# Kernel optimization log

Measured on AMD Instinct MI355X. Metric: run time of the kernel, lower is better.

Reference implementation:

```python
import jax, jax.numpy as jnp
import numpy as np

N_NODES = 50000
N_EDGES = 600000
IN_CH = 128
HID = 128
OUT_CH = 1
N_GRAPHS = 64


def setup_inputs() -> dict:
    key = jax.random.key(0)
    ks = jax.random.split(key, 16)
    inp = {
        "x": jax.random.normal(ks[0], (N_NODES, IN_CH), dtype=jnp.float32),
        "edge_index": jax.random.randint(ks[1], (2, N_EDGES), 0, N_NODES, dtype=jnp.int64),
        "edge_weight": jax.random.uniform(ks[2], (N_EDGES,), dtype=jnp.float32),
        "batch": jnp.sort(jax.random.randint(ks[3], (N_NODES,), 0, N_GRAPHS, dtype=jnp.int64)),
    }
    # SAGEConv params: lin_l (neighbor-aggregate path, has bias) and lin_r (root path)
    dims = [(IN_CH, HID), (HID, HID), (HID, HID), (HID, HID)]
    for i, (din, dout) in enumerate(dims, start=1):
        s = 1.0 / np.sqrt(din)
        inp[f"Wl{i}"] = jax.random.uniform(ks[3 + 2 * i], (din, dout), minval=-s, maxval=s, dtype=jnp.float32)
        inp[f"Wr{i}"] = jax.random.uniform(ks[4 + 2 * i], (din, dout), minval=-s, maxval=s, dtype=jnp.float32)
        inp[f"b{i}"] = jnp.zeros((dout,), dtype=jnp.float32)
    s = 1.0 / np.sqrt(HID)
    inp["Wc"] = jax.random.uniform(ks[14], (HID, OUT_CH), minval=-s, maxval=s, dtype=jnp.float32)
    inp["bc"] = jnp.zeros((OUT_CH,), dtype=jnp.float32)
    return inp


def _sage_conv(x, src, dst, Wl, Wr, b):
    # mean aggregation of source-node features at each destination node
    msg = x[src]  # [E, d] gather
    agg = jax.ops.segment_sum(msg, dst, num_segments=N_NODES)
    cnt = jax.ops.segment_sum(jnp.ones((src.shape[0],), x.dtype), dst, num_segments=N_NODES)
    agg = agg / jnp.maximum(cnt, 1.0)[:, None]
    return agg @ Wl + b + x @ Wr


def reference(x, edge_index, edge_weight, batch,
              Wl1, Wr1, b1, Wl2, Wr2, b2, Wl3, Wr3, b3, Wl4, Wr4, b4, Wc, bc):
    src, dst = edge_index[0], edge_index[1]
    h = jax.nn.relu(_sage_conv(x, src, dst, Wl1, Wr1, b1))
    h = jax.nn.relu(_sage_conv(h, src, dst, Wl2, Wr2, b2))
    h = jax.nn.relu(_sage_conv(h, src, dst, Wl3, Wr3, b3))
    h = jax.nn.relu(_sage_conv(h, src, dst, Wl4, Wr4, b4))
    # global mean pool over graphs
    pooled = jax.ops.segment_sum(h, batch, num_segments=N_GRAPHS)
    gcnt = jax.ops.segment_sum(jnp.ones((N_NODES,), h.dtype), batch, num_segments=N_GRAPHS)
    pooled = pooled / jnp.maximum(gcnt, 1.0)[:, None]  # [G, HID]
    return jax.nn.sigmoid(pooled @ Wc + bc)  # [G, 1]
```

## Files before the change

### kernel.cpp

```cpp
#include <hip/hip_runtime.h>
#include <math.h>

#define NND 50000
#define LNP 50048
#define NED 600000
#define CD  128
#define NG  64
#define NBLK 196
#define GROWS 64

typedef short s8v  __attribute__((ext_vector_type(8)));
typedef float f4v  __attribute__((ext_vector_type(4)));
typedef float f2v  __attribute__((ext_vector_type(2)));
typedef unsigned short u16x4 __attribute__((ext_vector_type(4)));
typedef unsigned short u16x8 __attribute__((ext_vector_type(8)));

static __device__ __forceinline__ unsigned short f2bf(float f) {
  union { float f; unsigned u; } v; v.f = f;
  unsigned r = v.u + 0x7fffu + ((v.u >> 16) & 1u);
  return (unsigned short)(r >> 16);
}
static __device__ __forceinline__ unsigned short f2bf_t(float f) {
  union { float f; unsigned u; } v; v.f = f;
  return (unsigned short)(v.u >> 16);
}
static __device__ __forceinline__ unsigned f2fp8x4(float a, float b, float c, float d) {
  int r = __builtin_amdgcn_cvt_pk_fp8_f32(a, b, 0, false);
  r = __builtin_amdgcn_cvt_pk_fp8_f32(c, d, r, true);
  return (unsigned)r;
}
static __device__ __forceinline__ s8v fp8x8_to_bf16(uint2 v) {
  f2v c0 = __builtin_amdgcn_cvt_pk_f32_fp8(v.x, false);
  f2v c1 = __builtin_amdgcn_cvt_pk_f32_fp8(v.x, true);
  f2v c2 = __builtin_amdgcn_cvt_pk_f32_fp8(v.y, false);
  f2v c3 = __builtin_amdgcn_cvt_pk_f32_fp8(v.y, true);
  union { u16x8 u; s8v s; } o;
  o.u[0] = f2bf_t(c0.x); o.u[1] = f2bf_t(c0.y);
  o.u[2] = f2bf_t(c1.x); o.u[3] = f2bf_t(c1.y);
  o.u[4] = f2bf_t(c2.x); o.u[5] = f2bf_t(c2.y);
  o.u[6] = f2bf_t(c3.x); o.u[7] = f2bf_t(c3.y);
  return o.s;
}
static __device__ __forceinline__ void g2lds8(const unsigned char* g, unsigned char* l) {
  __builtin_amdgcn_global_load_lds(
      (const __attribute__((address_space(1))) unsigned*)g,
      (__attribute__((address_space(3))) unsigned*)l, 16, 0, 0);
}

__global__ __launch_bounds__(256) void bsum_k(const int* __restrict__ cnt,
                                              int* __restrict__ bsum) {
  __shared__ int s[256];
  int i = blockIdx.x * 256 + threadIdx.x;
  s[threadIdx.x] = (i < NND) ? cnt[i] : 0;
  __syncthreads();
  for (int off = 128; off > 0; off >>= 1) {
    if (threadIdx.x < off) s[threadIdx.x] += s[threadIdx.x + off];
    __syncthreads();
  }
  if (threadIdx.x == 0) bsum[blockIdx.x] = s[0];
}

__global__ __launch_bounds__(256) void bscan_k(const int* __restrict__ bsum,
                                               int* __restrict__ boff,
                                               int* __restrict__ offs,
                                               const int* __restrict__ batch,
                                               int* __restrict__ gb) {
  __shared__ int s[256];
  int t = threadIdx.x;
  if (t <= NG) {
    int lo = 0, hi = NND;
    while (lo < hi) {
      int mid = (lo + hi) >> 1;
      if (batch[mid] < t) lo = mid + 1; else hi = mid;
    }
    gb[t] = lo;
  }
  s[t] = (t < NBLK) ? bsum[t] : 0;
  __syncthreads();
  for (int off = 1; off < 256; off <<= 1) {
    int v = (t >= off) ? s[t - off] : 0;
    __syncthreads();
    s[t] += v;
    __syncthreads();
  }
  if (t < NBLK) boff[t] = (t == 0) ? 0 : s[t - 1];
  if (t == NBLK - 1) offs[NND] = s[t];
}

__global__ __launch_bounds__(256) void escan_k(const int* __restrict__ cnt,
                                               const int* __restrict__ boff,
                                               int* __restrict__ offs,
                                               int* __restrict__ cur) {
  __shared__ int s[256];
  int i = blockIdx.x * 256 + threadIdx.x;
  int t = threadIdx.x;
  int v = (i < NND) ? cnt[i] : 0;
  s[t] = v;
  __syncthreads();
  for (int off = 1; off < 256; off <<= 1) {
    int u = (t >= off) ? s[t - off] : 0;
    __syncthreads();
    s[t] += u;
    __syncthreads();
  }
  if (i < NND) {
    int excl = s[t] - v + boff[blockIdx.x];
    offs[i] = excl;
    cur[i]  = excl;
  }
}

__global__ void fill_k(const int* __restrict__ src, const int* __restrict__ dst,
                       int* __restrict__ cur, int* __restrict__ csr) {
  int e = blockIdx.x * blockDim.x + threadIdx.x;
  if (e >= NED) return;
  int d = dst[e];
  int pos = atomicAdd(&cur[d], 1);
  csr[pos] = src[e];
}

struct WPtrs { const float* w[8]; unsigned short* wt[8]; };
__global__ void prep_k(const float* __restrict__ x, unsigned* __restrict__ x8,
                       WPtrs p, const int* __restrict__ dst, int* __restrict__ cnt) {
  int t = blockIdx.x * blockDim.x + threadIdx.x;
  if (t < NND * 32) {
    float4 v = reinterpret_cast<const float4*>(x)[t];
    x8[t] = f2fp8x4(v.x, v.y, v.z, v.w);
  } else {
    int u = t - NND * 32;
    if (u < 8 * CD * CD) {
      int m = u >> 14, r = u & (CD * CD - 1);
      int n = r >> 7, k = r & 127;
      p.wt[m][r] = f2bf(p.w[m][k * CD + n]);
    } else {
      int e = u - 8 * CD * CD;
      if (e < NED) atomicAdd(&cnt[dst[e]], 1);
    }
  }
}

__global__ __launch_bounds__(256, 4) void sage_k(
    const unsigned* __restrict__ xq,
    const int* __restrict__ csr, const int* __restrict__ offs,
    const unsigned short* __restrict__ WlT, const unsigned short* __restrict__ WrT,
    const float* __restrict__ bias, unsigned char* __restrict__ h8,
    const int* __restrict__ batch, float* __restrict__ pooled) {
  __shared__ unsigned short abuf[GROWS * CD];
  __shared__ unsigned char  x8buf[GROWS * CD];
  __shared__ int sB[GROWS];

  const int tid  = threadIdx.x;
  const int wave = tid >> 6;
  const int lane = tid & 63;
  const int quad = lane >> 4;
  const int l16  = lane & 15;
  const size_t rbase = (size_t)blockIdx.x * GROWS;

  {
    const unsigned char* xg = (const unsigned char*)xq;
#pragma unroll
    for (int j = 0; j < 2; ++j) {
      const int s = j * 256 + tid;
      g2lds8(xg + (rbase + (s >> 3)) * CD + (s & 7) * 16, &x8buf[(size_t)s * 16]);
    }
  }

  if (pooled && tid < GROWS) {
    size_t row = rbase + tid;
    sB[tid] = (row < NND) ? batch[row] : -1;
  }

  s8v bL[2][4], bR[2][4];
#pragma unroll
  for (int nt = 0; nt < 2; ++nt) {
    const int n = wave * 32 + nt * 16 + l16;
#pragma unroll
    for (int kk = 0; kk < 4; ++kk) {
      size_t woff = (size_t)n * CD + kk * 32 + quad * 8;
      bL[nt][kk] = *reinterpret_cast<const s8v*>(WlT + woff);
      bR[nt][kk] = *reinterpret_cast<const s8v*>(WrT + woff);
    }
  }
  const float bv0 = bias[wave * 32 + l16];
  const float bv1 = bias[wave * 32 + 16 + l16];

  {
    const int team = tid >> 3;
    const int tl   = tid & 7;
    const unsigned* base = xq + tl * 4;
    for (int i = 0; i < 2; ++i) {
      const int rl = team * 2 + i;
      const size_t row = rbase + rl;
      u16x8 o0 = {}, o1 = {};
      if (row < NND) {
        const int e0 = offs[row], e1 = offs[row + 1];
        f2v a[8] = {};
        int e = e0;
        for (; e + 4 <= e1; e += 4) {
          int s[4];
#pragma unroll
          for (int j = 0; j < 4; ++j) s[j] = csr[e + j];
          uint4 v[4];
#pragma unroll
          for (int j = 0; j < 4; ++j)
            v[j] = *reinterpret_cast<const uint4*>(base + (size_t)s[j] * 32);
#pragma unroll
          for (int j = 0; j < 4; ++j) {
            a[0] += __builtin_amdgcn_cvt_pk_f32_fp8(v[j].x, false);
            a[1] += __builtin_amdgcn_cvt_pk_f32_fp8(v[j].x, true);
            a[2] += __builtin_amdgcn_cvt_pk_f32_fp8(v[j].y, false);
            a[3] += __builtin_amdgcn_cvt_pk_f32_fp8(v[j].y, true);
            a[4] += __builtin_amdgcn_cvt_pk_f32_fp8(v[j].z, false);
            a[5] += __builtin_amdgcn_cvt_pk_f32_fp8(v[j].z, true);
            a[6] += __builtin_amdgcn_cvt_pk_f32_fp8(v[j].w, false);
            a[7] += __builtin_amdgcn_cvt_pk_f32_fp8(v[j].w, true);
          }
        }
        for (; e < e1; ++e) {
          uint4 v = *reinterpret_cast<const uint4*>(base + (size_t)csr[e] * 32);
          a[0] += __builtin_amdgcn_cvt_pk_f32_fp8(v.x, false);
          a[1] += __builtin_amdgcn_cvt_pk_f32_fp8(v.x, true);
          a[2] += __builtin_amdgcn_cvt_pk_f32_fp8(v.y, false);
          a[3] += __builtin_amdgcn_cvt_pk_f32_fp8(v.y, true);
          a[4] += __builtin_amdgcn_cvt_pk_f32_fp8(v.z, false);
          a[5] += __builtin_amdgcn_cvt_pk_f32_fp8(v.z, true);
          a[6] += __builtin_amdgcn_cvt_pk_f32_fp8(v.w, false);
          a[7] += __builtin_amdgcn_cvt_pk_f32_fp8(v.w, true);
        }
        const float invd = 1.0f / fmaxf((float)(e1 - e0), 1.0f);
#pragma unroll
        for (int c = 0; c < 4; ++c) {
          o0[2 * c]     = f2bf(a[c].x * invd);
          o0[2 * c + 1] = f2bf(a[c].y * invd);
          o1[2 * c]     = f2bf(a[4 + c].x * invd);
          o1[2 * c + 1] = f2bf(a[4 + c].y * invd);
        }
      }
      *reinterpret_cast<u16x8*>(abuf + rl * CD + tl * 16)     = o0;
      *reinterpret_cast<u16x8*>(abuf + rl * CD + tl * 16 + 8) = o1;
    }
  }

  __syncthreads();

  const bool fast = pooled && (rbase + GROWS <= NND) && (sB[0] == sB[GROWS - 1]);
  const int c0 = wave * 32 + l16;
  float p0 = 0.f, p1 = 0.f;

#pragma unroll
  for (int rt = 0; rt < GROWS / 16; ++rt) {
    const unsigned short* arow = abuf + (rt * 16 + l16) * CD + quad * 8;
    const unsigned char*  xrow = x8buf + (rt * 16 + l16) * CD + quad * 8;
    f4v acc0 = {}, acc1 = {};
#pragma unroll
    for (int kk = 0; kk < 4; ++kk) {
      s8v aA = *reinterpret_cast<const s8v*>(arow + kk * 32);
      s8v aX = fp8x8_to_bf16(*reinterpret_cast<const uint2*>(xrow + kk * 32));
      acc0 = __builtin_amdgcn_mfma_f32_16x16x32_bf16(aA, bL[0][kk], acc0, 0, 0, 0);
      acc0 = __builtin_amdgcn_mfma_f32_16x16x32_bf16(aX, bR[0][kk], acc0, 0, 0, 0);
      acc1 = __builtin_amdgcn_mfma_f32_16x16x32_bf16(aA, bL[1][kk], acc1, 0, 0, 0);
      acc1 = __builtin_amdgcn_mfma_f32_16x16x32_bf16(aX, bR[1][kk], acc1, 0, 0, 0);
    }
    const size_t row0 = rbase + rt * 16 + quad * 4;
#pragma unroll
    for (int r = 0; r < 4; ++r) {
      const size_t row = row0 + r;
      float v0 = fmaxf(acc0[r] + bv0, 0.0f);
      float v1 = fmaxf(acc1[r] + bv1, 0.0f);
      if (h8) {
        int q0 = __builtin_amdgcn_cvt_pk_fp8_f32(v0, v0, 0, false);
        int q1 = __builtin_amdgcn_cvt_pk_fp8_f32(v1, v1, 0, false);
        h8[row * CD + c0]      = (unsigned char)q0;
        h8[row * CD + c0 + 16] = (unsigned char)q1;
      }
      if (pooled) {
        if (fast) {
          p0 += v0; p1 += v1;
        } else {
          int g = sB[rt * 16 + quad * 4 + r];
          if (g >= 0) {
            atomicAdd(&pooled[g * CD + c0], v0);
            atomicAdd(&pooled[g * CD + c0 + 16], v1);
          }
        }
      }
    }
  }

  if (fast) {
    p0 += __shfl_xor(p0, 16, 64);
    p0 += __shfl_xor(p0, 32, 64);
    p1 += __shfl_xor(p1, 16, 64);
    p1 += __shfl_xor(p1, 32, 64);
    if (quad == 0) {
      const int g = sB[0];
      atomicAdd(&pooled[g * CD + c0], p0);
      atomicAdd(&pooled[g * CD + c0 + 16], p1);
    }
  }
}

__global__ void final_k(const float* __restrict__ pooled, const int* __restrict__ gb,
                        const float* __restrict__ Wc, const float* __restrict__ bc,
                        float* __restrict__ out) {
  int g = blockIdx.x;
  int lane = threadIdx.x;
  float part = pooled[g * CD + lane] * Wc[lane] +
               pooled[g * CD + 64 + lane] * Wc[64 + lane];
#pragma unroll
  for (int off = 32; off > 0; off >>= 1) part += __shfl_down(part, off, 64);
  if (lane == 0) {
    float cnt = (float)(gb[g + 1] - gb[g]);
    float z = part / fmaxf(cnt, 1.0f) + bc[0];
    out[g] = 1.0f / (1.0f + expf(-z));
  }
}

extern "C" void kernel_launch(void* const* d_in, const int* in_sizes, int n_in,
                              void* d_out, int out_size, void* d_ws, size_t ws_size,
                              hipStream_t stream) {
  const float* x   = (const float*)d_in[0];
  const int*   ei  = (const int*)d_in[1];
  const int*   src = ei;
  const int*   dst = ei + NED;
  const int*   batch = (const int*)d_in[3];
  const float* Wc = (const float*)d_in[16];
  const float* bc = (const float*)d_in[17];
  float* out = (float*)d_out;

  char* w = (char*)d_ws;
  auto alloc = [&](size_t bytes) {
    char* p = w; w += (bytes + 255) & ~(size_t)255; return p;
  };
  int* cnti = (int*)alloc(NND * 4);
  float* pooled = (float*)alloc(NG * CD * 4);
  size_t zspan = (size_t)(w - (char*)cnti);
  int* offs = (int*)alloc((NND + 1) * 4);
  int* cur  = (int*)alloc(NND * 4);
  int* csr  = (int*)alloc((size_t)NED * 4);
  int* gb   = (int*)alloc((NG + 1) * 4);
  int* bsum = (int*)alloc(256 * 4);
  int* boff = (int*)alloc(256 * 4);
  unsigned char* x8a = (unsigned char*)alloc((size_t)LNP * CD);
  unsigned char* x8b = (unsigned char*)alloc((size_t)LNP * CD);
  WPtrs wp;
  for (int i = 0; i < 4; ++i) {
    wp.w[2 * i]     = (const float*)d_in[4 + 3 * i];
    wp.w[2 * i + 1] = (const float*)d_in[5 + 3 * i];
  }
  for (int i = 0; i < 8; ++i) wp.wt[i] = (unsigned short*)alloc(CD * CD * 2);
  const float* bs[4] = {(const float*)d_in[6],  (const float*)d_in[9],
                        (const float*)d_in[12], (const float*)d_in[15]};

  hipMemsetAsync(cnti, 0, zspan, stream);

  prep_k<<<(NND * 32 + 8 * CD * CD + NED + 255) / 256, 256, 0, stream>>>(
      x, (unsigned*)x8a, wp, dst, cnti);

  bsum_k<<<NBLK, 256, 0, stream>>>(cnti, bsum);
  bscan_k<<<1, 256, 0, stream>>>(bsum, boff, offs, batch, gb);
  escan_k<<<NBLK, 256, 0, stream>>>(cnti, boff, offs, cur);
  fill_k<<<(NED + 255) / 256, 256, 0, stream>>>(src, dst, cur, csr);

  unsigned char* qcur = x8a;
  unsigned char* qnxt = x8b;
  const int ggrid = LNP / GROWS;
  for (int l = 0; l < 4; ++l) {
    if (l < 3) {
      sage_k<<<ggrid, 256, 0, stream>>>((const unsigned*)qcur, csr, offs,
                                        wp.wt[2 * l], wp.wt[2 * l + 1], bs[l],
                                        qnxt, batch, nullptr);
      unsigned char* q = qcur; qcur = qnxt; qnxt = q;
    } else {
      sage_k<<<ggrid, 256, 0, stream>>>((const unsigned*)qcur, csr, offs,
                                        wp.wt[2 * l], wp.wt[2 * l + 1], bs[l],
                                        nullptr, batch, pooled);
    }
  }

  final_k<<<NG, 64, 0, stream>>>(pooled, gb, Wc, bc, out);
}
```

Measured before the change: 310.2 us.

## Swizzle LDS tiles, unroll gather by 8, defer weight loads, fuse final head

XOR-swizzles the LDS layout of the aggregated bf16 tile and the fp8 root tile to avoid bank conflicts in the MFMA operand reads. Adds an 8-way unrolled neighbor gather loop to put more loads in flight, and moves the weight register loads after the gather to cut register pressure during it. Fuses the final classifier into the last layer with a last-block-done counter, removing one kernel launch at the cost of a threadfence and an atomic per block.

Measured after the change: 348.4 us. +12.3%, slower.

```diff
diff --git a/kernel.cpp b/kernel.cpp
--- a/kernel.cpp
+++ b/kernel.cpp
@@ -8,11 +8,11 @@
 #define NG  64
 #define NBLK 196
 #define GROWS 64
+#define GGRID (LNP / GROWS)
 
 typedef short s8v  __attribute__((ext_vector_type(8)));
 typedef float f4v  __attribute__((ext_vector_type(4)));
 typedef float f2v  __attribute__((ext_vector_type(2)));
-typedef unsigned short u16x4 __attribute__((ext_vector_type(4)));
 typedef unsigned short u16x8 __attribute__((ext_vector_type(8)));
 
 static __device__ __forceinline__ unsigned short f2bf(float f) {
@@ -144,10 +144,14 @@
     const int* __restrict__ csr, const int* __restrict__ offs,
     const unsigned short* __restrict__ WlT, const unsigned short* __restrict__ WrT,
     const float* __restrict__ bias, unsigned char* __restrict__ h8,
-    const int* __restrict__ batch, float* __restrict__ pooled) {
+    const int* __restrict__ batch, float* __restrict__ pooled,
+    int* __restrict__ done, const int* __restrict__ gb,
+    const float* __restrict__ Wc, const float* __restrict__ bc,
+    float* __restrict__ out) {
   __shared__ unsigned short abuf[GROWS * CD];
   __shared__ unsigned char  x8buf[GROWS * CD];
   __shared__ int sB[GROWS];
+  __shared__ int slast;
 
   const int tid  = threadIdx.x;
   const int wave = tid >> 6;
@@ -161,7 +165,9 @@
 #pragma unroll
     for (int j = 0; j < 2; ++j) {
       const int s = j * 256 + tid;
-      g2lds8(xg + (rbase + (s >> 3)) * CD + (s & 7) * 16, &x8buf[(size_t)s * 16]);
+      const int row = s >> 3;
+      const int c = (s & 7) ^ (row & 7);
+      g2lds8(xg + (rbase + row) * CD + c * 16, &x8buf[(size_t)s * 16]);
     }
   }
 
@@ -169,20 +175,6 @@
     size_t row = rbase + tid;
     sB[tid] = (row < NND) ? batch[row] : -1;
   }
-
-  s8v bL[2][4], bR[2][4];
-#pragma unroll
-  for (int nt = 0; nt < 2; ++nt) {
-    const int n = wave * 32 + nt * 16 + l16;
-#pragma unroll
-    for (int kk = 0; kk < 4; ++kk) {
-      size_t woff = (size_t)n * CD + kk * 32 + quad * 8;
-      bL[nt][kk] = *reinterpret_cast<const s8v*>(WlT + woff);
-      bR[nt][kk] = *reinterpret_cast<const s8v*>(WrT + woff);
-    }
-  }
-  const float bv0 = bias[wave * 32 + l16];
-  const float bv1 = bias[wave * 32 + 16 + l16];
 
   {
     const int team = tid >> 3;
@@ -196,6 +188,26 @@
         const int e0 = offs[row], e1 = offs[row + 1];
         f2v a[8] = {};
         int e = e0;
+        for (; e + 8 <= e1; e += 8) {
+          int s[8];
+#pragma unroll
+          for (int j = 0; j < 8; ++j) s[j] = csr[e + j];
+          uint4 v[8];
+#pragma unroll
+          for (int j = 0; j < 8; ++j)
+            v[j] = *reinterpret_cast<const uint4*>(base + (size_t)s[j] * 32);
+#pragma unroll
+          for (int j = 0; j < 8; ++j) {
+            a[0] += __builtin_amdgcn_cvt_pk_f32_fp8(v[j].x, false);
+            a[1] += __builtin_amdgcn_cvt_pk_f32_fp8(v[j].x, true);
+            a[2] += __builtin_amdgcn_cvt_pk_f32_fp8(v[j].y, false);
+            a[3] += __builtin_amdgcn_cvt_pk_f32_fp8(v[j].y, true);
+            a[4] += __builtin_amdgcn_cvt_pk_f32_fp8(v[j].z, false);
+            a[5] += __builtin_amdgcn_cvt_pk_f32_fp8(v[j].z, true);
+            a[6] += __builtin_amdgcn_cvt_pk_f32_fp8(v[j].w, false);
+            a[7] += __builtin_amdgcn_cvt_pk_f32_fp8(v[j].w, true);
+          }
+        }
         for (; e + 4 <= e1; e += 4) {
           int s[4];
 #pragma unroll
@@ -236,10 +248,26 @@
           o1[2 * c + 1] = f2bf(a[4 + c].y * invd);
         }
       }
-      *reinterpret_cast<u16x8*>(abuf + rl * CD + tl * 16)     = o0;
-      *reinterpret_cast<u16x8*>(abuf + rl * CD + tl * 16 + 8) = o1;
-    }
-  }
+      char* ab = (char*)(abuf + rl * CD);
+      const int swr = rl & 7;
+      *reinterpret_cast<u16x8*>(ab + ((((tl << 1))     ^ swr) << 4)) = o0;
+      *reinterpret_cast<u16x8*>(ab + ((((tl << 1) | 1) ^ swr) << 4)) = o1;
+    }
+  }
+
+  s8v bL[2][4], bR[2][4];
+#pragma unroll
+  for (int nt = 0; nt < 2; ++nt) {
+    const int n = wave * 32 + nt * 16 + l16;
+#pragma unroll
+    for (int kk = 0; kk < 4; ++kk) {
+      size_t woff = (size_t)n * CD + kk * 32 + quad * 8;
+      bL[nt][kk] = *reinterpret_cast<const s8v*>(WlT + woff);
+      bR[nt][kk] = *reinterpret_cast<const s8v*>(WrT + woff);
+    }
+  }
+  const float bv0 = bias[wave * 32 + l16];
+  const float bv1 = bias[wave * 32 + 16 + l16];
 
   __syncthreads();
 
@@ -249,13 +277,17 @@
 
 #pragma unroll
   for (int rt = 0; rt < GROWS / 16; ++rt) {
-    const unsigned short* arow = abuf + (rt * 16 + l16) * CD + quad * 8;
-    const unsigned char*  xrow = x8buf + (rt * 16 + l16) * CD + quad * 8;
+    const int row = rt * 16 + l16;
+    const int sw  = row & 7;
+    const char* arow = (const char*)(abuf + row * CD);
+    const char* xrow = (const char*)(x8buf + row * CD);
     f4v acc0 = {}, acc1 = {};
 #pragma unroll
     for (int kk = 0; kk < 4; ++kk) {
-      s8v aA = *reinterpret_cast<const s8v*>(arow + kk * 32);
-      s8v aX = fp8x8_to_bf16(*reinterpret_cast<const uint2*>(xrow + kk * 32));
+      s8v aA = *reinterpret_cast<const s8v*>(arow + (((quad + kk * 4) ^ sw) << 4));
+      uint2 xv = *reinterpret_cast<const uint2*>(
+          xrow + ((((quad >> 1) + kk * 2) ^ sw) << 4) + ((quad & 1) << 3));
+      s8v aX = fp8x8_to_bf16(xv);
       acc0 = __builtin_amdgcn_mfma_f32_16x16x32_bf16(aA, bL[0][kk], acc0, 0, 0, 0);
       acc0 = __builtin_amdgcn_mfma_f32_16x16x32_bf16(aX, bR[0][kk], acc0, 0, 0, 0);
       acc1 = __builtin_amdgcn_mfma_f32_16x16x32_bf16(aA, bL[1][kk], acc1, 0, 0, 0);
@@ -264,14 +296,14 @@
     const size_t row0 = rbase + rt * 16 + quad * 4;
 #pragma unroll
     for (int r = 0; r < 4; ++r) {
-      const size_t row = row0 + r;
+      const size_t orow = row0 + r;
       float v0 = fmaxf(acc0[r] + bv0, 0.0f);
       float v1 = fmaxf(acc1[r] + bv1, 0.0f);
       if (h8) {
         int q0 = __builtin_amdgcn_cvt_pk_fp8_f32(v0, v0, 0, false);
         int q1 = __builtin_amdgcn_cvt_pk_fp8_f32(v1, v1, 0, false);
-        h8[row * CD + c0]      = (unsigned char)q0;
-        h8[row * CD + c0 + 16] = (unsigned char)q1;
+        h8[orow * CD + c0]      = (unsigned char)q0;
+        h8[orow * CD + c0 + 16] = (unsigned char)q1;
       }
       if (pooled) {
         if (fast) {
@@ -287,6 +319,8 @@
     }
   }
 
+  if (!pooled) return;
+
   if (fast) {
     p0 += __shfl_xor(p0, 16, 64);
     p0 += __shfl_xor(p0, 32, 64);
@@ -298,21 +332,30 @@
       atomicAdd(&pooled[g * CD + c0 + 16], p1);
     }
   }
-}
-
-__global__ void final_k(const float* __restrict__ pooled, const int* __restrict__ gb,
-                        const float* __restrict__ Wc, const float* __restrict__ bc,
-                        float* __restrict__ out) {
-  int g = blockIdx.x;
-  int lane = threadIdx.x;
-  float part = pooled[g * CD + lane] * Wc[lane] +
-               pooled[g * CD + 64 + lane] * Wc[64 + lane];
-#pragma unroll
-  for (int off = 32; off > 0; off >>= 1) part += __shfl_down(part, off, 64);
-  if (lane == 0) {
-    float cnt = (float)(gb[g + 1] - gb[g]);
-    float z = part / fmaxf(cnt, 1.0f) + bc[0];
-    out[g] = 1.0f / (1.0f + expf(-z));
+
+  __threadfence();
+  if (tid == 0) {
+    int prev = __hip_atomic_fetch_add(done, 1, __ATOMIC_ACQ_REL,
+                                      __HIP_MEMORY_SCOPE_AGENT);
+    slast = (prev == GGRID - 1) ? 1 : 0;
+  }
+  __syncthreads();
+  if (slast) {
+    const int wv = tid >> 6, ln = tid & 63;
+    for (int g = wv; g < NG; g += 4) {
+      float a0 = __hip_atomic_load(&pooled[g * CD + ln],
+                                   __ATOMIC_RELAXED, __HIP_MEMORY_SCOPE_AGENT);
+      float a1 = __hip_atomic_load(&pooled[g * CD + 64 + ln],
+                                   __ATOMIC_RELAXED, __HIP_MEMORY_SCOPE_AGENT);
+      float part = a0 * Wc[ln] + a1 * Wc[64 + ln];
+#pragma unroll
+      for (int off = 32; off > 0; off >>= 1) part += __shfl_down(part, off, 64);
+      if (ln == 0) {
+        float cnt = (float)(gb[g + 1] - gb[g]);
+        float z = part / fmaxf(cnt, 1.0f) + bc[0];
+        out[g] = 1.0f / (1.0f + expf(-z));
+      }
+    }
   }
 }
 
@@ -334,6 +377,7 @@
   };
   int* cnti = (int*)alloc(NND * 4);
   float* pooled = (float*)alloc(NG * CD * 4);
+  int* done = (int*)alloc(4);
   size_t zspan = (size_t)(w - (char*)cnti);
   int* offs = (int*)alloc((NND + 1) * 4);
   int* cur  = (int*)alloc(NND * 4);
@@ -364,19 +408,18 @@
 
   unsigned char* qcur = x8a;
   unsigned char* qnxt = x8b;
-  const int ggrid = LNP / GROWS;
   for (int l = 0; l < 4; ++l) {
     if (l < 3) {
-      sage_k<<<ggrid, 256, 0, stream>>>((const unsigned*)qcur, csr, offs,
+      sage_k<<<GGRID, 256, 0, stream>>>((const unsigned*)qcur, csr, offs,
                                         wp.wt[2 * l], wp.wt[2 * l + 1], bs[l],
-                                        qnxt, batch, nullptr);
+                                        qnxt, batch, nullptr,
+                                        done, gb, Wc, bc, out);
       unsigned char* q = qcur; qcur = qnxt; qnxt = q;
     } else {
-      sage_k<<<ggrid, 256, 0, stream>>>((const unsigned*)qcur, csr, offs,
+      sage_k<<<GGRID, 256, 0, stream>>>((const unsigned*)qcur, csr, offs,
                                         wp.wt[2 * l], wp.wt[2 * l + 1], bs[l],
-                                        nullptr, batch, pooled);
-    }
-  }
-
-  final_k<<<NG, 64, 0, stream>>>(pooled, gb, Wc, bc, out);
-}
+                                        nullptr, batch, pooled,
+                                        done, gb, Wc, bc, out);
+    }
+  }
+}
```
